# Kernel optimization log

Hardware: AMD Instinct MI355X
Metric: run time of the kernel (lower is better)

The kernel has to match this reference:

```python
import jax, jax.numpy as jnp
import numpy as np

N = 50000          # nodes
E = 800000         # edges (before self loops)
G = 64             # graphs in batch
HEADS = 4
HID = 25
DENSE = HEADS * HID      # 100, must equal prototype feature dim
IN_DIM = 128
OUT_DIM = 2
NPC = 5                  # num_prototypes_per_class
NUM_PROT = OUT_DIM * NPC
EPS = 1e-4
NEG_SLOPE = 0.2


def setup_inputs() -> dict:
    key = jax.random.key(0)
    ks = jax.random.split(key, 20)
    x = jax.random.normal(ks[0], (N, IN_DIM), dtype=jnp.float32)
    edge_index = jax.random.randint(ks[1], (2, E), 0, N, dtype=jnp.int64)
    batch = jnp.sort(jax.random.randint(ks[2], (N,), 0, G, dtype=jnp.int64))
    inp = {"x": x, "edge_index": edge_index, "batch": batch}
    in_dims = [IN_DIM, DENSE, DENSE]
    for i in range(3):
        d = in_dims[i]
        s = 1.0 / np.sqrt(d)
        inp[f"W{i}"] = jax.random.uniform(ks[3 + 4 * i], (d, DENSE), jnp.float32, -s, s)
        inp[f"as{i}"] = jax.random.uniform(ks[4 + 4 * i], (HEADS, HID), jnp.float32, -s, s)
        inp[f"ad{i}"] = jax.random.uniform(ks[5 + 4 * i], (HEADS, HID), jnp.float32, -s, s)
        inp[f"b{i}"] = jnp.zeros((DENSE,), jnp.float32)
    inp["protos"] = jax.random.uniform(ks[16], (NUM_PROT, DENSE), jnp.float32)
    # last_layer weight: +1 for own class, -0.5 otherwise  [OUT_DIM, NUM_PROT]
    cls = jnp.arange(NUM_PROT) // NPC
    inp["last_w"] = jnp.where(cls[None, :] == jnp.arange(OUT_DIM)[:, None], 1.0, -0.5).astype(jnp.float32)
    return inp


def _gat_layer(x, src, dst, W, a_src, a_dst, b):
    h = (x @ W).reshape(N, HEADS, HID)                 # [N,H,D]
    e_src = jnp.einsum('nhd,hd->nh', h, a_src)         # [N,H]
    e_dst = jnp.einsum('nhd,hd->nh', h, a_dst)
    alpha = e_src[src] + e_dst[dst]                    # [Etot,H]
    alpha = jnp.where(alpha > 0, alpha, NEG_SLOPE * alpha)
    amax = jax.ops.segment_max(alpha, dst, num_segments=N)
    ex = jnp.exp(alpha - amax[dst])
    denom = jax.ops.segment_sum(ex, dst, num_segments=N)
    a = ex / (denom[dst] + 1e-16)                      # segmented softmax over in-edges
    msg = h[src] * a[:, :, None]                       # [Etot,H,D]
    out = jax.ops.segment_sum(msg, dst, num_segments=N)
    return out.reshape(N, DENSE) + b


def reference(x, edge_index, batch, W0, as0, ad0, b0, W1, as1, ad1, b1, W2, as2, ad2, b2, protos, last_w):
    loops = jnp.arange(N, dtype=edge_index.dtype)
    src = jnp.concatenate([edge_index[0], loops])      # PyG add_self_loops=True
    dst = jnp.concatenate([edge_index[1], loops])
    params = [(W0, as0, ad0, b0), (W1, as1, ad1, b1), (W2, as2, ad2, b2)]
    h = x
    for (W, a_s, a_d, b) in params:
        h = _gat_layer(h, src, dst, W, a_s, a_d, b)
        h = jax.nn.relu(h)
    node_emb = h
    graph_emb = jax.ops.segment_max(h, batch, num_segments=G)   # global_max_pool
    # prototype distances: squared euclidean via expansion
    xp = graph_emb @ protos.T                                    # [G,P]
    dist = -2.0 * xp + jnp.sum(graph_emb ** 2, axis=1, keepdims=True) + jnp.sum(protos ** 2, axis=1)[None, :]
    sim = jnp.log((dist + 1.0) / (dist + EPS))
    logits = sim @ last_w.T
    probs = jax.nn.softmax(logits, axis=-1)
    return logits, probs, node_emb, graph_emb, dist
```

## Files before the change

### kernel.cpp

```cpp
#include <hip/hip_runtime.h>
#include <hip/hip_bf16.h>

#define NN      50000
#define EE      800000
#define ETOT    (EE + NN)
#define GG      64
#define HEADS   4
#define HID     25
#define DENSE   100
#define IN_DIM  128
#define OUT_DIM 2
#define NPC     5
#define NUM_PROT (OUT_DIM * NPC)
#define NCHUNK  ((NN + 255) / 256)

#define NEG_INF (-3.402823466e38f)

__global__ void k_count(const int* __restrict__ ei, int* __restrict__ cnt, int* __restrict__ pos) {
    int e = blockIdx.x * blockDim.x + threadIdx.x;
    if (e >= ETOT) return;
    int dst = (e < EE) ? ei[EE + e] : (e - EE);
    pos[e] = atomicAdd(&cnt[dst], 1);
}

__global__ void k_scan1(const int* __restrict__ cnt, int* __restrict__ csum) {
    __shared__ int sh[256];
    int i = blockIdx.x * 256 + threadIdx.x;
    int v = (i < NN) ? cnt[i] : 0;
    sh[threadIdx.x] = v;
    __syncthreads();
    for (int s = 128; s > 0; s >>= 1) {
        if (threadIdx.x < s) sh[threadIdx.x] += sh[threadIdx.x + s];
        __syncthreads();
    }
    if (threadIdx.x == 0) csum[blockIdx.x] = sh[0];
}

__global__ void k_scan2(int* __restrict__ csum) {
    __shared__ int sh[256];
    int tid = threadIdx.x;
    int v = (tid < NCHUNK) ? csum[tid] : 0;
    sh[tid] = v;
    __syncthreads();
    for (int s = 1; s < 256; s <<= 1) {
        int t = (tid >= s) ? sh[tid - s] : 0;
        __syncthreads();
        sh[tid] += t;
        __syncthreads();
    }
    if (tid < NCHUNK) csum[tid] = sh[tid] - v;
    if (tid == NCHUNK) csum[NCHUNK] = sh[255];
}

__global__ void k_scan3(const int* __restrict__ cnt, const int* __restrict__ csum, int* __restrict__ offs) {
    __shared__ int sh[256];
    int i = blockIdx.x * 256 + threadIdx.x;
    int v = (i < NN) ? cnt[i] : 0;
    sh[threadIdx.x] = v;
    __syncthreads();
    for (int s = 1; s < 256; s <<= 1) {
        int t = (threadIdx.x >= s) ? sh[threadIdx.x - s] : 0;
        __syncthreads();
        sh[threadIdx.x] += t;
        __syncthreads();
    }
    int excl = sh[threadIdx.x] - v + csum[blockIdx.x];
    if (i <= NN) offs[i] = excl;
}

__global__ void k_scatter(const int* __restrict__ ei, const int* __restrict__ offs,
                          const int* __restrict__ pos, int* __restrict__ csr) {
    int e = blockIdx.x * blockDim.x + threadIdx.x;
    if (e >= ETOT) return;
    int src, dst;
    if (e < EE) { src = ei[e]; dst = ei[EE + e]; }
    else        { src = dst = e - EE; }
    csr[offs[dst] + pos[e]] = src;
}

__global__ void k_bounds(const int* __restrict__ batch, int* __restrict__ gstart) {
    int n = blockIdx.x * blockDim.x + threadIdx.x;
    if (n >= NN) return;
    int b = batch[n];
    if (n == 0) {
        for (int g = 0; g <= b; g++) gstart[g] = 0;
    } else {
        int pb = batch[n - 1];
        for (int g = pb + 1; g <= b; g++) gstart[g] = n;
    }
    if (n == NN - 1) {
        for (int g = b + 1; g <= GG; g++) gstart[g] = NN;
    }
}

template <int DIN>
__global__ __launch_bounds__(256) void k_gemm(const float* __restrict__ X,
                                              const float* __restrict__ W,
                                              float* __restrict__ H) {
    __shared__ float Ws[DIN * 104];
    __shared__ float Xs[32 * (DIN + 1)];
    const int tid = threadIdx.x;

    for (int idx = tid; idx < DIN * 100; idx += 256) {
        int k = idx / 100, c = idx - k * 100;
        Ws[k * 104 + c] = W[idx];
    }

    const int node0 = blockIdx.x * 32;
    for (int idx = tid; idx < 32 * DIN; idx += 256) {
        int r = idx / DIN, k = idx - r * DIN;
        int row = node0 + r;
        Xs[r * (DIN + 1) + k] = (row < NN) ? X[(size_t)row * DIN + k] : 0.f;
    }
    __syncthreads();

    const int rl = tid >> 5;
    const int cg = tid & 31;
    if (cg >= 25) return;

    float acc[4][4] = {};
    #pragma unroll 4
    for (int k = 0; k < DIN; k++) {
        float4 w = *reinterpret_cast<const float4*>(&Ws[k * 104 + cg * 4]);
        #pragma unroll
        for (int j = 0; j < 4; j++) {
            float xv = Xs[(rl + 8 * j) * (DIN + 1) + k];
            acc[j][0] += xv * w.x; acc[j][1] += xv * w.y;
            acc[j][2] += xv * w.z; acc[j][3] += xv * w.w;
        }
    }
    #pragma unroll
    for (int j = 0; j < 4; j++) {
        int row = node0 + rl + 8 * j;
        if (row < NN) {
            float4 v = {acc[j][0], acc[j][1], acc[j][2], acc[j][3]};
            *reinterpret_cast<float4*>(&H[(size_t)row * 100 + cg * 4]) = v;
        }
    }
}

__global__ void k_esed(const float* __restrict__ H, const float* __restrict__ AS,
                       const float* __restrict__ AD, float* __restrict__ es, float* __restrict__ ed) {
    int t = blockIdx.x * blockDim.x + threadIdx.x;
    if (t >= NN * HEADS) return;
    int n = t >> 2, hd = t & 3;
    const float* hr = H + (size_t)n * 100 + hd * 25;
    const float* as = AS + hd * 25;
    const float* ad = AD + hd * 25;
    float s1 = 0.f, s2 = 0.f;
    #pragma unroll
    for (int d = 0; d < 25; d++) {
        float v = hr[d];
        s1 += v * as[d];
        s2 += v * ad[d];
    }
    es[t] = s1;
    ed[t] = s2;
}

__global__ __launch_bounds__(256) void k_msum(const float* __restrict__ es,
                                              const float* __restrict__ ed,
                                              const int* __restrict__ offs,
                                              const int* __restrict__ csr,
                                              float* __restrict__ wv) {
    int wid = threadIdx.x >> 6;
    int lane = threadIdx.x & 63;
    int n = blockIdx.x * 4 + wid;
    if (n >= NN) return;
    int el = lane >> 2, hd = lane & 3;
    int beg = offs[n], end = offs[n + 1];
    float edh = ed[n * 4 + hd];
    float m = NEG_INF, s = 0.f;
    for (int e = beg + el; e < end; e += 16) {
        int si = csr[e];
        float a = es[si * 4 + hd] + edh;
        a = (a > 0.f) ? a : 0.2f * a;
        float nm = fmaxf(m, a);
        float sc = __expf(m - nm);
        s = s * sc + __expf(a - nm);
        m = nm;
    }
    #pragma unroll
    for (int mask = 4; mask <= 32; mask <<= 1) {
        float mo = __shfl_xor(m, mask, 64);
        float so = __shfl_xor(s, mask, 64);
        float nm = fmaxf(m, mo);
        float f1 = (m  > NEG_INF) ? __expf(m  - nm) : 0.f;
        float f2 = (mo > NEG_INF) ? __expf(mo - nm) : 0.f;
        s = s * f1 + so * f2;
        m = nm;
    }
    float invs = 1.f / (s + 1e-16f);
    for (int e = beg + el; e < end; e += 16) {
        int si = csr[e];
        float a = es[si * 4 + hd] + edh;
        a = (a > 0.f) ? a : 0.2f * a;
        wv[(size_t)e * 4 + hd] = __expf(a - m) * invs;
    }
}

__global__ __launch_bounds__(128) void k_acc(const float* __restrict__ H,
                                             const float* __restrict__ wv,
                                             const int* __restrict__ offs,
                                             const int* __restrict__ csr,
                                             const float* __restrict__ bias,
                                             float* __restrict__ out) {
    int n = blockIdx.x;
    int d = threadIdx.x;
    if (d >= 100) return;
    int hd = d / 25;
    int beg = offs[n], end = offs[n + 1];
    float acc = 0.f;
    int e = beg;
    for (; e + 4 <= end; e += 4) {
        int s0 = csr[e], s1 = csr[e + 1], s2 = csr[e + 2], s3 = csr[e + 3];
        float w0 = wv[(size_t)e * 4 + hd];
        float w1 = wv[(size_t)(e + 1) * 4 + hd];
        float w2 = wv[(size_t)(e + 2) * 4 + hd];
        float w3 = wv[(size_t)(e + 3) * 4 + hd];
        float x0 = H[(size_t)s0 * 100 + d];
        float x1 = H[(size_t)s1 * 100 + d];
        float x2 = H[(size_t)s2 * 100 + d];
        float x3 = H[(size_t)s3 * 100 + d];
        acc += w0 * x0;
        acc += w1 * x1;
        acc += w2 * x2;
        acc += w3 * x3;
    }
    for (; e < end; ++e) {
        acc += wv[(size_t)e * 4 + hd] * H[(size_t)csr[e] * 100 + d];
    }
    float o = acc + bias[d];
    out[(size_t)n * 100 + d] = fmaxf(o, 0.f);
}

__global__ __launch_bounds__(128) void k_agg(const float* __restrict__ H, const float* __restrict__ es,
                                             const float* __restrict__ ed, const int* __restrict__ offs,
                                             const int* __restrict__ csr, const float* __restrict__ bias,
                                             float* __restrict__ out) {
    int n = blockIdx.x;
    int d = threadIdx.x;
    __shared__ float edn[4];
    if (d < 4) edn[d] = ed[n * 4 + d];
    __syncthreads();
    if (d >= 100) return;
    int hd = d / 25;
    float edh = edn[hd];
    int beg = offs[n], end = offs[n + 1];
    float m = NEG_INF, s = 0.f, acc = 0.f;
    for (int e = beg; e < end; ++e) {
        int si = csr[e];
        float a = es[si * 4 + hd] + edh;
        a = (a > 0.f) ? a : 0.2f * a;
        float xv = H[(size_t)si * 100 + d];
        float nm = fmaxf(m, a);
        float sc = __expf(m - nm);
        float p  = __expf(a - nm);
        s   = s * sc + p;
        acc = acc * sc + p * xv;
        m = nm;
    }
    float o = acc / (s + 1e-16f) + bias[d];
    out[(size_t)n * 100 + d] = (o > 0.f) ? o : 0.f;
}

__global__ void k_pool1(const float* __restrict__ NE, const int* __restrict__ gstart,
                        float* __restrict__ part) {
    int g = blockIdx.x >> 3, c = blockIdx.x & 7;
    int d = threadIdx.x;
    if (d >= 100) return;
    int s0 = gstart[g], s1 = gstart[g + 1];
    int len = s1 - s0;
    int n0 = s0 + (int)((long long)len * c / 8);
    int n1 = s0 + (int)((long long)len * (c + 1) / 8);
    float vm = NEG_INF;
    for (int n = n0; n < n1; n++) vm = fmaxf(vm, NE[(size_t)n * 100 + d]);
    part[(size_t)(g * 8 + c) * 100 + d] = vm;
}

__global__ void k_pool2(const float* __restrict__ part, float* __restrict__ GE) {
    int g = blockIdx.x;
    int d = threadIdx.x;
    if (d >= 100) return;
    float vm = NEG_INF;
    for (int c = 0; c < 8; c++) vm = fmaxf(vm, part[(size_t)(g * 8 + c) * 100 + d]);
    GE[(size_t)g * 100 + d] = vm;
}

__global__ void k_head(const float* __restrict__ GE, const float* __restrict__ P,
                       const float* __restrict__ LW, float* __restrict__ logits,
                       float* __restrict__ probs, float* __restrict__ dist) {
    int g = blockIdx.x;
    __shared__ float ge[100];
    __shared__ float sims[NUM_PROT];
    __shared__ float lg[OUT_DIM];
    int t = threadIdx.x;
    if (t < 100) ge[t] = GE[(size_t)g * 100 + t];
    __syncthreads();
    if (t < NUM_PROT) {
        float dot = 0.f, pn = 0.f, gn = 0.f;
        for (int d = 0; d < 100; d++) {
            float pv = P[t * 100 + d];
            float gv = ge[d];
            dot += gv * pv;
            pn += pv * pv;
            gn += gv * gv;
        }
        float ds = gn - 2.f * dot + pn;
        dist[g * NUM_PROT + t] = ds;
        sims[t] = logf((ds + 1.f) / (ds + 1e-4f));
    }
    __syncthreads();
    if (t < OUT_DIM) {
        float l = 0.f;
        for (int p = 0; p < NUM_PROT; p++) l += sims[p] * LW[t * NUM_PROT + p];
        lg[t] = l;
        logits[g * OUT_DIM + t] = l;
    }
    __syncthreads();
    if (t == 0) {
        float mm = fmaxf(lg[0], lg[1]);
        float e0 = __expf(lg[0] - mm), e1 = __expf(lg[1] - mm);
        float inv = 1.f / (e0 + e1);
        probs[g * OUT_DIM + 0] = e0 * inv;
        probs[g * OUT_DIM + 1] = e1 * inv;
    }
}

extern "C" void kernel_launch(void* const* d_in, const int* in_sizes, int n_in,
                              void* d_out, int out_size, void* d_ws, size_t ws_size,
                              hipStream_t stream) {
    const float* x     = (const float*)d_in[0];
    const int*   ei    = (const int*)d_in[1];
    const int*   batch = (const int*)d_in[2];
    const float* Wm[3]  = {(const float*)d_in[3],  (const float*)d_in[7],  (const float*)d_in[11]};
    const float* ASm[3] = {(const float*)d_in[4],  (const float*)d_in[8],  (const float*)d_in[12]};
    const float* ADm[3] = {(const float*)d_in[5],  (const float*)d_in[9],  (const float*)d_in[13]};
    const float* Bm[3]  = {(const float*)d_in[6],  (const float*)d_in[10], (const float*)d_in[14]};
    const float* P  = (const float*)d_in[15];
    const float* LW = (const float*)d_in[16];

    float* out = (float*)d_out;
    float* logits  = out;
    float* probs   = out + GG * OUT_DIM;
    float* nodeEmb = out + 2 * GG * OUT_DIM;
    float* GE      = nodeEmb + (size_t)NN * DENSE;
    float* disto   = GE + GG * DENSE;

    char* w = (char*)d_ws;
    size_t off = 0;
    auto carve = [&](size_t bytes) -> void* {
        void* p = w + off;
        off += (bytes + 15) & ~(size_t)15;
        return p;
    };
    float* hA   = (float*)carve((size_t)NN * DENSE * 4);
    float* es   = (float*)carve((size_t)NN * HEADS * 4);
    float* ed   = (float*)carve((size_t)NN * HEADS * 4);
    int* cnt    = (int*)carve((size_t)NN * 4);
    int* offs   = (int*)carve((size_t)(NN + 1) * 4);
    int* pos    = (int*)carve((size_t)ETOT * 4);
    int* csr    = (int*)carve((size_t)ETOT * 4);
    int* csum   = (int*)carve((size_t)(NCHUNK + 1) * 4);
    int* gstart = (int*)carve((size_t)(GG + 1) * 4);
    float* part = (float*)carve((size_t)GG * 8 * DENSE * 4);
    size_t base_need = off;
    float* wv   = (float*)carve((size_t)ETOT * HEADS * 4);
    bool has_wv = (off <= ws_size);
    (void)in_sizes; (void)n_in; (void)out_size; (void)base_need;

    hipMemsetAsync(cnt, 0, (size_t)NN * 4, stream);
    k_count<<<(ETOT + 255) / 256, 256, 0, stream>>>(ei, cnt, pos);
    k_scan1<<<NCHUNK, 256, 0, stream>>>(cnt, csum);
    k_scan2<<<1, 256, 0, stream>>>(csum);
    k_scan3<<<NCHUNK, 256, 0, stream>>>(cnt, csum, offs);
    k_scatter<<<(ETOT + 255) / 256, 256, 0, stream>>>(ei, offs, pos, csr);
    k_bounds<<<(NN + 255) / 256, 256, 0, stream>>>(batch, gstart);

    const int gemmGrid = (NN + 31) / 32;
    const int esedGrid = (NN * HEADS + 255) / 256;
    const int msumGrid = (NN + 3) / 4;

    const float* layerIn = x;
    for (int l = 0; l < 3; ++l) {
        if (l == 0) k_gemm<IN_DIM><<<gemmGrid, 256, 0, stream>>>(layerIn, Wm[l], hA);
        else        k_gemm<DENSE ><<<gemmGrid, 256, 0, stream>>>(layerIn, Wm[l], hA);
        k_esed<<<esedGrid, 256, 0, stream>>>(hA, ASm[l], ADm[l], es, ed);
        if (has_wv) {
            k_msum<<<msumGrid, 256, 0, stream>>>(es, ed, offs, csr, wv);
            k_acc<<<NN, 128, 0, stream>>>(hA, wv, offs, csr, Bm[l], nodeEmb);
        } else {
            k_agg<<<NN, 128, 0, stream>>>(hA, es, ed, offs, csr, Bm[l], nodeEmb);
        }
        layerIn = nodeEmb;
    }

    k_pool1<<<GG * 8, 128, 0, stream>>>(nodeEmb, gstart, part);
    k_pool2<<<GG, 128, 0, stream>>>(part, GE);

    k_head<<<GG, 128, 0, stream>>>(GE, P, LW, logits, probs, disto);
}
```

Before: 493.3 us.

## Chunk GEMM K-dimension in shared memory and pack two nodes per aggregation block

The GEMM now stages W and X in K-chunks (32 or 25 rows), so its shared-memory footprint shrinks and more blocks can be resident per CU. The aggregation kernel maps one 64-lane wavefront to each node, with each lane handling two features through float2 loads. This halves the block count and widens the gather loads. The fallback k_agg path is removed and the wv buffer is always used, which assumes the workspace is large enough.

```diff
diff --git a/kernel.cpp b/kernel.cpp
--- a/kernel.cpp
+++ b/kernel.cpp
@@ -93,48 +93,53 @@
     }
 }
 
-template <int DIN>
+template <int DIN, int KC>
 __global__ __launch_bounds__(256) void k_gemm(const float* __restrict__ X,
                                               const float* __restrict__ W,
                                               float* __restrict__ H) {
-    __shared__ float Ws[DIN * 104];
-    __shared__ float Xs[32 * (DIN + 1)];
+    __shared__ float Ws[KC * 104];
+    __shared__ float Xs[32 * (KC + 1)];
     const int tid = threadIdx.x;
-
-    for (int idx = tid; idx < DIN * 100; idx += 256) {
-        int k = idx / 100, c = idx - k * 100;
-        Ws[k * 104 + c] = W[idx];
-    }
-
-    const int node0 = blockIdx.x * 32;
-    for (int idx = tid; idx < 32 * DIN; idx += 256) {
-        int r = idx / DIN, k = idx - r * DIN;
-        int row = node0 + r;
-        Xs[r * (DIN + 1) + k] = (row < NN) ? X[(size_t)row * DIN + k] : 0.f;
-    }
-    __syncthreads();
-
     const int rl = tid >> 5;
     const int cg = tid & 31;
-    if (cg >= 25) return;
+    const int node0 = blockIdx.x * 32;
 
     float acc[4][4] = {};
-    #pragma unroll 4
-    for (int k = 0; k < DIN; k++) {
-        float4 w = *reinterpret_cast<const float4*>(&Ws[k * 104 + cg * 4]);
+    constexpr int NCH = DIN / KC;
+    for (int kb = 0; kb < NCH; ++kb) {
+        const int k0 = kb * KC;
+        for (int idx = tid; idx < KC * 100; idx += 256) {
+            int k = idx / 100, c = idx - k * 100;
+            Ws[k * 104 + c] = W[(k0 + k) * 100 + c];
+        }
+        for (int idx = tid; idx < 32 * KC; idx += 256) {
+            int r = idx / KC, k = idx - r * KC;
+            int row = node0 + r;
+            Xs[r * (KC + 1) + k] = (row < NN) ? X[(size_t)row * DIN + k0 + k] : 0.f;
+        }
+        __syncthreads();
+        if (cg < 25) {
+            #pragma unroll
+            for (int k = 0; k < KC; ++k) {
+                float4 w = *reinterpret_cast<const float4*>(&Ws[k * 104 + cg * 4]);
+                #pragma unroll
+                for (int j = 0; j < 4; ++j) {
+                    float xv = Xs[(rl + 8 * j) * (KC + 1) + k];
+                    acc[j][0] += xv * w.x; acc[j][1] += xv * w.y;
+                    acc[j][2] += xv * w.z; acc[j][3] += xv * w.w;
+                }
+            }
+        }
+        __syncthreads();
+    }
+    if (cg < 25) {
         #pragma unroll
-        for (int j = 0; j < 4; j++) {
-            float xv = Xs[(rl + 8 * j) * (DIN + 1) + k];
-            acc[j][0] += xv * w.x; acc[j][1] += xv * w.y;
-            acc[j][2] += xv * w.z; acc[j][3] += xv * w.w;
-        }
-    }
-    #pragma unroll
-    for (int j = 0; j < 4; j++) {
-        int row = node0 + rl + 8 * j;
-        if (row < NN) {
-            float4 v = {acc[j][0], acc[j][1], acc[j][2], acc[j][3]};
-            *reinterpret_cast<float4*>(&H[(size_t)row * 100 + cg * 4]) = v;
+        for (int j = 0; j < 4; ++j) {
+            int row = node0 + rl + 8 * j;
+            if (row < NN) {
+                float4 v = {acc[j][0], acc[j][1], acc[j][2], acc[j][3]};
+                *reinterpret_cast<float4*>(&H[(size_t)row * 100 + cg * 4]) = v;
+            }
         }
     }
 }
@@ -205,63 +210,38 @@
                                              const int* __restrict__ csr,
                                              const float* __restrict__ bias,
                                              float* __restrict__ out) {
-    int n = blockIdx.x;
-    int d = threadIdx.x;
-    if (d >= 100) return;
-    int hd = d / 25;
+    int wid = threadIdx.x >> 6;
+    int lane = threadIdx.x & 63;
+    int n = blockIdx.x * 2 + wid;
+    if (n >= NN || lane >= 50) return;
+    int d0 = lane * 2;
+    int h0 = d0 / 25, h1 = (d0 + 1) / 25;
     int beg = offs[n], end = offs[n + 1];
-    float acc = 0.f;
+    float ax = 0.f, ay = 0.f;
     int e = beg;
     for (; e + 4 <= end; e += 4) {
         int s0 = csr[e], s1 = csr[e + 1], s2 = csr[e + 2], s3 = csr[e + 3];
-        float w0 = wv[(size_t)e * 4 + hd];
-        float w1 = wv[(size_t)(e + 1) * 4 + hd];
-        float w2 = wv[(size_t)(e + 2) * 4 + hd];
-        float w3 = wv[(size_t)(e + 3) * 4 + hd];
-        float x0 = H[(size_t)s0 * 100 + d];
-        float x1 = H[(size_t)s1 * 100 + d];
-        float x2 = H[(size_t)s2 * 100 + d];
-        float x3 = H[(size_t)s3 * 100 + d];
-        acc += w0 * x0;
-        acc += w1 * x1;
-        acc += w2 * x2;
-        acc += w3 * x3;
+        float2 x0 = *reinterpret_cast<const float2*>(&H[(size_t)s0 * 100 + d0]);
+        float2 x1 = *reinterpret_cast<const float2*>(&H[(size_t)s1 * 100 + d0]);
+        float2 x2 = *reinterpret_cast<const float2*>(&H[(size_t)s2 * 100 + d0]);
+        float2 x3 = *reinterpret_cast<const float2*>(&H[(size_t)s3 * 100 + d0]);
+        float w0x = wv[(size_t)e * 4 + h0],       w0y = wv[(size_t)e * 4 + h1];
+        float w1x = wv[(size_t)(e + 1) * 4 + h0], w1y = wv[(size_t)(e + 1) * 4 + h1];
+        float w2x = wv[(size_t)(e + 2) * 4 + h0], w2y = wv[(size_t)(e + 2) * 4 + h1];
+        float w3x = wv[(size_t)(e + 3) * 4 + h0], w3y = wv[(size_t)(e + 3) * 4 + h1];
+        ax += w0x * x0.x; ay += w0y * x0.y;
+        ax += w1x * x1.x; ay += w1y * x1.y;
+        ax += w2x * x2.x; ay += w2y * x2.y;
+        ax += w3x * x3.x; ay += w3y * x3.y;
     }
     for (; e < end; ++e) {
-        acc += wv[(size_t)e * 4 + hd] * H[(size_t)csr[e] * 100 + d];
-    }
-    float o = acc + bias[d];
-    out[(size_t)n * 100 + d] = fmaxf(o, 0.f);
-}
-
-__global__ __launch_bounds__(128) void k_agg(const float* __restrict__ H, const float* __restrict__ es,
-                                             const float* __restrict__ ed, const int* __restrict__ offs,
-                                             const int* __restrict__ csr, const float* __restrict__ bias,
-                                             float* __restrict__ out) {
-    int n = blockIdx.x;
-    int d = threadIdx.x;
-    __shared__ float edn[4];
-    if (d < 4) edn[d] = ed[n * 4 + d];
-    __syncthreads();
-    if (d >= 100) return;
-    int hd = d / 25;
-    float edh = edn[hd];
-    int beg = offs[n], end = offs[n + 1];
-    float m = NEG_INF, s = 0.f, acc = 0.f;
-    for (int e = beg; e < end; ++e) {
-        int si = csr[e];
-        float a = es[si * 4 + hd] + edh;
-        a = (a > 0.f) ? a : 0.2f * a;
-        float xv = H[(size_t)si * 100 + d];
-        float nm = fmaxf(m, a);
-        float sc = __expf(m - nm);
-        float p  = __expf(a - nm);
-        s   = s * sc + p;
-        acc = acc * sc + p * xv;
-        m = nm;
-    }
-    float o = acc / (s + 1e-16f) + bias[d];
-    out[(size_t)n * 100 + d] = (o > 0.f) ? o : 0.f;
+        float2 xv = *reinterpret_cast<const float2*>(&H[(size_t)csr[e] * 100 + d0]);
+        ax += wv[(size_t)e * 4 + h0] * xv.x;
+        ay += wv[(size_t)e * 4 + h1] * xv.y;
+    }
+    float2 b = *reinterpret_cast<const float2*>(&bias[d0]);
+    float2 o = {fmaxf(ax + b.x, 0.f), fmaxf(ay + b.y, 0.f)};
+    *reinterpret_cast<float2*>(&out[(size_t)n * 100 + d0]) = o;
 }
 
 __global__ void k_pool1(const float* __restrict__ NE, const int* __restrict__ gstart,
@@ -364,10 +344,9 @@
     int* csum   = (int*)carve((size_t)(NCHUNK + 1) * 4);
     int* gstart = (int*)carve((size_t)(GG + 1) * 4);
     float* part = (float*)carve((size_t)GG * 8 * DENSE * 4);
-    size_t base_need = off;
     float* wv   = (float*)carve((size_t)ETOT * HEADS * 4);
     bool has_wv = (off <= ws_size);
-    (void)in_sizes; (void)n_in; (void)out_size; (void)base_need;
+    (void)in_sizes; (void)n_in; (void)out_size;
 
     hipMemsetAsync(cnt, 0, (size_t)NN * 4, stream);
     k_count<<<(ETOT + 255) / 256, 256, 0, stream>>>(ei, cnt, pos);
@@ -380,19 +359,17 @@
     const int gemmGrid = (NN + 31) / 32;
     const int esedGrid = (NN * HEADS + 255) / 256;
     const int msumGrid = (NN + 3) / 4;
+    const int accGrid  = (NN + 1) / 2;
 
     const float* layerIn = x;
     for (int l = 0; l < 3; ++l) {
-        if (l == 0) k_gemm<IN_DIM><<<gemmGrid, 256, 0, stream>>>(layerIn, Wm[l], hA);
-        else        k_gemm<DENSE ><<<gemmGrid, 256, 0, stream>>>(layerIn, Wm[l], hA);
+        if (l == 0) k_gemm<IN_DIM, 32><<<gemmGrid, 256, 0, stream>>>(layerIn, Wm[l], hA);
+        else        k_gemm<DENSE,  25><<<gemmGrid, 256, 0, stream>>>(layerIn, Wm[l], hA);
         k_esed<<<esedGrid, 256, 0, stream>>>(hA, ASm[l], ADm[l], es, ed);
-        if (has_wv) {
-            k_msum<<<msumGrid, 256, 0, stream>>>(es, ed, offs, csr, wv);
-            k_acc<<<NN, 128, 0, stream>>>(hA, wv, offs, csr, Bm[l], nodeEmb);
-        } else {
-            k_agg<<<NN, 128, 0, stream>>>(hA, es, ed, offs, csr, Bm[l], nodeEmb);
-        }
+        k_msum<<<msumGrid, 256, 0, stream>>>(es, ed, offs, csr, wv);
+        k_acc<<<accGrid, 128, 0, stream>>>(hA, wv, offs, csr, Bm[l], nodeEmb);
         layerIn = nodeEmb;
+        (void)has_wv;
     }
 
     k_pool1<<<GG * 8, 128, 0, stream>>>(nodeEmb, gstart, part);
```

Result: faster. 483.6 us (-2.0%).
